# Kernel optimization log

Measured on AMD Instinct MI355X. Metric: run time of the kernel, lower is better.

## Reference

```python
import jax, jax.numpy as jnp
import numpy as np

N = 8192

def setup_inputs() -> dict:
    key = jax.random.key(0)
    k1, k2, k3 = jax.random.split(key, 3)
    hazard_pred = jax.random.normal(k1, (N, 1), dtype=jnp.float32)
    survtime = jax.random.uniform(k2, (N,), dtype=jnp.float32)
    censor = jax.random.uniform(k3, (N,), dtype=jnp.float32)
    return {"hazard_pred": hazard_pred, "survtime": survtime, "censor": censor}

def reference(hazard_pred, survtime, censor):
    # R_mat[i, j] = 1 if survtime[j] >= survtime[i] else 0  (risk set mask)
    theta = hazard_pred.reshape(-1)                          # [n]
    R_mat = (survtime[None, :] >= survtime[:, None]).astype(theta.dtype)  # [n, n]
    exp_theta = jnp.exp(theta)                               # [n]
    risk_sum = jnp.sum(exp_theta[None, :] * R_mat, axis=1)   # [n]
    loss_cox = -jnp.mean((theta - jnp.log(risk_sum)) * censor)
    return loss_cox
```

## Files before the change

### kernel.cpp

```cpp
#include <hip/hip_runtime.h>
#include <math.h>


#define T_BLK 1024
#define I_PER_BLK 32
#define NP 32

__global__ __launch_bounds__(T_BLK) void cox_loss_kernel(
    const float* __restrict__ theta,
    const float* __restrict__ survtime,
    const float* __restrict__ censor,
    float* __restrict__ out,
    float* __restrict__ acc,
    unsigned int* __restrict__ ticket,
    int n, int nblocks)
{
    __shared__ float s_exp[8192];
    __shared__ float s_time[8192];

    const int tid = threadIdx.x;

    const int nvec = n >> 2;
    const float4* th4 = (const float4*)theta;
    const float4* st4 = (const float4*)survtime;
    for (int v = tid; v < nvec; v += T_BLK) {
        float4 t = th4[v];
        float4 s = st4[v];
        int j = v << 2;
        s_exp[j + 0] = expf(t.x);
        s_exp[j + 1] = expf(t.y);
        s_exp[j + 2] = expf(t.z);
        s_exp[j + 3] = expf(t.w);
        s_time[j + 0] = s.x;
        s_time[j + 1] = s.y;
        s_time[j + 2] = s.z;
        s_time[j + 3] = s.w;
    }
    __syncthreads();

    const int i_local = tid & (I_PER_BLK - 1);
    const int p       = tid >> 5;
    const int i       = blockIdx.x * I_PER_BLK + i_local;
    const float ti    = s_time[i];

    const int ch = n / NP;
    const float4* e4 = (const float4*)(s_exp + p * ch);
    const float4* t4 = (const float4*)(s_time + p * ch);
    float sum = 0.0f;
    #pragma unroll 4
    for (int k = 0; k < ch / 4; ++k) {
        float4 e = e4[k];
        float4 s = t4[k];
        sum += (s.x >= ti) ? e.x : 0.0f;
        sum += (s.y >= ti) ? e.y : 0.0f;
        sum += (s.z >= ti) ? e.z : 0.0f;
        sum += (s.w >= ti) ? e.w : 0.0f;
    }

    __syncthreads();
    s_exp[tid] = sum;
    __syncthreads();

    if (tid < I_PER_BLK) {
        float rs = 0.0f;
        #pragma unroll
        for (int q = 0; q < NP; ++q)
            rs += s_exp[q * I_PER_BLK + tid];

        float contrib = (theta[i] - logf(rs)) * censor[i];

        #pragma unroll
        for (int off = 16; off > 0; off >>= 1)
            contrib += __shfl_down(contrib, off);

        if (tid == 0) {
            atomicAdd(acc, contrib);
            __threadfence();
            unsigned int old = atomicAdd(ticket, 1u);
            if (old == (unsigned int)(nblocks - 1)) {
                float total = atomicAdd(acc, 0.0f);
                out[0] = -total / (float)n;
            }
        }
    }
}

extern "C" void kernel_launch(void* const* d_in, const int* in_sizes, int n_in,
                              void* d_out, int out_size, void* d_ws, size_t ws_size,
                              hipStream_t stream) {
    const float* theta    = (const float*)d_in[0];
    const float* survtime = (const float*)d_in[1];
    const float* censor   = (const float*)d_in[2];
    float* out = (float*)d_out;

    const int n = in_sizes[1];

    float* acc            = (float*)d_ws;
    unsigned int* ticket  = (unsigned int*)((char*)d_ws + sizeof(float));

    hipMemsetAsync(d_ws, 0, 2 * sizeof(float), stream);

    const int nblocks = n / I_PER_BLK;
    cox_loss_kernel<<<nblocks, T_BLK, 0, stream>>>(
        theta, survtime, censor, out, acc, ticket, n, nblocks);
}
```

Baseline: 73.82 us.

## Register-tile 8 rows per thread and replace atomic ticket with finalize kernel

Each thread now computes 8 rows against a 32-element chunk of j, so every shared-memory float4 load is reused across 8 comparisons instead of one. This is meant to cut LDS traffic per comparison. A two-stage shared reduction replaces the single 32-way sum. The memset and the atomic ticket are dropped in favour of per-block partials and a second single-block finalize kernel, which adds a launch but removes the atomics and the memset. The finalize kernel only reads up to 256 partials, so correctness depends on n/32 <= 256 (true for N=8192).

```diff
diff --git a/kernel.cpp b/kernel.cpp
--- a/kernel.cpp
+++ b/kernel.cpp
@@ -2,28 +2,27 @@
 #include <math.h>
 
 
-#define T_BLK 1024
-#define I_PER_BLK 32
-#define NP 32
+#define TBLK 1024
+#define ROWS_PER_BLK 32
+#define RPT 8
+#define JP 32
 
-__global__ __launch_bounds__(T_BLK) void cox_loss_kernel(
+__global__ __launch_bounds__(TBLK) void cox_main(
     const float* __restrict__ theta,
     const float* __restrict__ survtime,
     const float* __restrict__ censor,
-    float* __restrict__ out,
-    float* __restrict__ acc,
-    unsigned int* __restrict__ ticket,
-    int n, int nblocks)
+    float* __restrict__ block_partials,
+    int n)
 {
     __shared__ float s_exp[8192];
     __shared__ float s_time[8192];
 
     const int tid = threadIdx.x;
+    const int b   = blockIdx.x;
 
-    const int nvec = n >> 2;
     const float4* th4 = (const float4*)theta;
     const float4* st4 = (const float4*)survtime;
-    for (int v = tid; v < nvec; v += T_BLK) {
+    for (int v = tid; v < (n >> 2); v += TBLK) {
         float4 t = th4[v];
         float4 s = st4[v];
         int j = v << 2;
@@ -38,51 +37,85 @@
     }
     __syncthreads();
 
-    const int i_local = tid & (I_PER_BLK - 1);
-    const int p       = tid >> 5;
-    const int i       = blockIdx.x * I_PER_BLK + i_local;
-    const float ti    = s_time[i];
+    const int ig    = tid & 3;
+    const int p     = tid >> 2;
+    const int row0  = ig * RPT;
+    const int ibase = b * ROWS_PER_BLK;
 
-    const int ch = n / NP;
-    const float4* e4 = (const float4*)(s_exp + p * ch);
-    const float4* t4 = (const float4*)(s_time + p * ch);
-    float sum = 0.0f;
-    #pragma unroll 4
-    for (int k = 0; k < ch / 4; ++k) {
+    float ti[RPT], acc[RPT];
+    #pragma unroll
+    for (int r = 0; r < RPT; ++r) {
+        ti[r]  = s_time[ibase + row0 + r];
+        acc[r] = 0.0f;
+    }
+
+    const float4* e4 = (const float4*)s_exp  + p * (JP / 4);
+    const float4* t4 = (const float4*)s_time + p * (JP / 4);
+    #pragma unroll
+    for (int k = 0; k < JP / 4; ++k) {
         float4 e = e4[k];
-        float4 s = t4[k];
-        sum += (s.x >= ti) ? e.x : 0.0f;
-        sum += (s.y >= ti) ? e.y : 0.0f;
-        sum += (s.z >= ti) ? e.z : 0.0f;
-        sum += (s.w >= ti) ? e.w : 0.0f;
+        float4 t = t4[k];
+        #pragma unroll
+        for (int r = 0; r < RPT; ++r) {
+            float tr = ti[r];
+            acc[r] += (t.x >= tr) ? e.x : 0.0f;
+            acc[r] += (t.y >= tr) ? e.y : 0.0f;
+            acc[r] += (t.z >= tr) ? e.z : 0.0f;
+            acc[r] += (t.w >= tr) ? e.w : 0.0f;
+        }
     }
 
     __syncthreads();
-    s_exp[tid] = sum;
+    #pragma unroll
+    for (int r = 0; r < RPT; ++r)
+        s_exp[p * ROWS_PER_BLK + row0 + r] = acc[r];
     __syncthreads();
 
-    if (tid < I_PER_BLK) {
+    {
+        const int il = tid & 31;
+        const int q  = tid >> 5;
+        float s = 0.0f;
+        #pragma unroll
+        for (int m = 0; m < 8; ++m)
+            s += s_exp[(q * 8 + m) * ROWS_PER_BLK + il];
+        s_time[q * ROWS_PER_BLK + il] = s;
+    }
+    __syncthreads();
+
+    if (tid < ROWS_PER_BLK) {
         float rs = 0.0f;
         #pragma unroll
-        for (int q = 0; q < NP; ++q)
-            rs += s_exp[q * I_PER_BLK + tid];
+        for (int q = 0; q < 32; ++q)
+            rs += s_time[q * ROWS_PER_BLK + tid];
 
+        const int i = ibase + tid;
         float contrib = (theta[i] - logf(rs)) * censor[i];
 
         #pragma unroll
         for (int off = 16; off > 0; off >>= 1)
             contrib += __shfl_down(contrib, off);
 
-        if (tid == 0) {
-            atomicAdd(acc, contrib);
-            __threadfence();
-            unsigned int old = atomicAdd(ticket, 1u);
-            if (old == (unsigned int)(nblocks - 1)) {
-                float total = atomicAdd(acc, 0.0f);
-                out[0] = -total / (float)n;
-            }
-        }
+        if (tid == 0)
+            block_partials[b] = contrib;
     }
+}
+
+__global__ __launch_bounds__(256) void cox_finalize(
+    const float* __restrict__ partials,
+    float* __restrict__ out,
+    int nblocks, int n)
+{
+    const int t = threadIdx.x;
+    float v = (t < nblocks) ? partials[t] : 0.0f;
+    #pragma unroll
+    for (int off = 32; off > 0; off >>= 1)
+        v += __shfl_down(v, off);
+
+    __shared__ float s[4];
+    if ((t & 63) == 0) s[t >> 6] = v;
+    __syncthreads();
+    if (t == 0)
+        out[0] = -(s[0] + s[1] + s[2] + s[3]) / (float)n;
 }
 
 extern "C" void kernel_launch(void* const* d_in, const int* in_sizes, int n_in,
@@ -94,13 +127,11 @@
     float* out = (float*)d_out;
 
     const int n = in_sizes[1];
+    const int nblocks = n / ROWS_PER_BLK;
 
-    float* acc            = (float*)d_ws;
-    unsigned int* ticket  = (unsigned int*)((char*)d_ws + sizeof(float));
+    float* block_partials = (float*)d_ws;
 
-    hipMemsetAsync(d_ws, 0, 2 * sizeof(float), stream);
-
-    const int nblocks = n / I_PER_BLK;
-    cox_loss_kernel<<<nblocks, T_BLK, 0, stream>>>(
-        theta, survtime, censor, out, acc, ticket, n, nblocks);
+    cox_main<<<nblocks, TBLK, 0, stream>>>(theta, survtime, censor,
+                                           block_partials, n);
+    cox_finalize<<<1, 256, 0, stream>>>(block_partials, out, nblocks, n);
 }
```

New measurement: 65.52 us. -11.2%, faster.
